# Kernel optimization log

Measured on AMD Instinct MI355X. Metric: run time of the kernel, lower is better.

## Reference

```python
import jax, jax.numpy as jnp
import numpy as np
from jax import lax

EPS = 1e-5

def _conv(x, w, b, pad):
    # NCHW conv, stride 1, symmetric padding `pad`
    y = lax.conv_general_dilated(x, w, window_strides=(1, 1),
                                 padding=[(pad, pad), (pad, pad)],
                                 dimension_numbers=('NCHW', 'OIHW', 'NCHW'))
    return y + b[None, :, None, None]

def _bn(x, gamma, beta):
    # BatchNorm2d, training mode: batch statistics over (N,H,W)
    mean = jnp.mean(x, axis=(0, 2, 3), keepdims=True)
    var = jnp.var(x, axis=(0, 2, 3), keepdims=True)
    return gamma[None, :, None, None] * (x - mean) * lax.rsqrt(var + EPS) + beta[None, :, None, None]

def setup_inputs() -> dict:
    key = jax.random.key(0)
    ks = jax.random.split(key, 8)
    B, C, H, W = 4, 256, 64, 64
    OC = 256
    s3 = 1.0 / np.sqrt(C * 9)
    s1 = 1.0 / np.sqrt(C)
    return {
        'x': jax.random.normal(ks[0], (B, C, H, W), jnp.float32),
        'Wq': jax.random.normal(ks[1], (OC, C, 3, 3), jnp.float32) * s3,
        'bq': jnp.zeros((OC,), jnp.float32),
        'gq': jnp.ones((OC,), jnp.float32),
        'betaq': jnp.zeros((OC,), jnp.float32),
        'Wk': jax.random.normal(ks[2], (OC, C, 1, 1), jnp.float32) * s1,
        'bk': jnp.zeros((OC,), jnp.float32),
        'gk': jnp.ones((OC,), jnp.float32),
        'betak': jnp.zeros((OC,), jnp.float32),
        'Wv': jax.random.normal(ks[3], (OC, C, 1, 1), jnp.float32) * s1,
        'bv': jnp.zeros((OC,), jnp.float32),
        'gv': jnp.ones((OC,), jnp.float32),
        'betav': jnp.zeros((OC,), jnp.float32),
    }

def reference(x, Wq, bq, gq, betaq, Wk, bk, gk, betak, Wv, bv, gv, betav):
    # Q: 3x3 conv, pad 1 -> (b, oc, h, w); K,V: 1x1 conv with pad 1 -> (b, oc, h+2, w+2)
    Q = _bn(_conv(x, Wq, bq, 1), gq, betaq)
    K = _bn(_conv(x, Wk, bk, 1), gk, betak)
    V = _bn(_conv(x, Wv, bv, 1), gv, betav)
    b, oc, oh, ow = Q.shape
    q = Q.reshape(b, oc, oh * ow)          # (b, c, q_tokens)
    k = K.reshape(b, oc, -1)               # (b, c, k_tokens)
    v = V.reshape(b, oc, -1)               # (b, c, k_tokens)
    scores = jnp.einsum('bck,bcq->bkq', k, q)      # (b, k_tokens, q_tokens)
    attn = jax.nn.softmax(scores, axis=1)          # softmax over key tokens (dim=1)
    out = jnp.einsum('bck,bkq->bcq', v, attn)      # (b, c, q_tokens)
    return out.reshape(b, oc, oh, ow)
```

## Files before the change

kernel.cpp:

```cpp
#include <hip/hip_runtime.h>


typedef unsigned short u16;
typedef _Float16 f16x8 __attribute__((ext_vector_type(8)));
typedef __attribute__((ext_vector_type(4))) float f32x4;

__device__ __forceinline__ u16 f2h(float f) {
  _Float16 h = (_Float16)f;
  return *(const u16*)&h;
}
__device__ __forceinline__ float bf2f(u16 h) {
  return __uint_as_float(((unsigned)h) << 16);
}
__device__ __forceinline__ float ldin(const void* p, size_t i, int f32) {
  return f32 ? ((const float*)p)[i] : bf2f(((const u16*)p)[i]);
}
__device__ __forceinline__ u16 f2bf(float f) {
  unsigned u = __float_as_uint(f);
  u += 0x7fffu + ((u >> 16) & 1u);
  return (u16)(u >> 16);
}
__device__ __forceinline__ void gld16(const void* g, void* l) {
  __builtin_amdgcn_global_load_lds(
      (const __attribute__((address_space(1))) unsigned int*)g,
      (__attribute__((address_space(3))) unsigned int*)l, 16, 0, 0);
}

__global__ __launch_bounds__(256) void k_detect(const unsigned* __restrict__ w,
                                                int* __restrict__ flag) {
  __shared__ int red[4];
  int tid = threadIdx.x, cnt = 0;
#pragma unroll
  for (int j = 0; j < 8; j++) {
    unsigned e = (w[tid + j * 8192] >> 7) & 0xFFu;
    cnt += (e >= 118u && e <= 127u) ? 1 : 0;
  }
#pragma unroll
  for (int off = 32; off; off >>= 1) cnt += __shfl_down(cnt, off);
  if ((tid & 63) == 0) red[tid >> 6] = cnt;
  __syncthreads();
  if (tid == 0)
    flag[0] = (red[0] + red[1] + red[2] + red[3] < 625) ? 1 : 0;
}

__global__ __launch_bounds__(256) void k_txp(const void* __restrict__ x,
                                             const int* __restrict__ flag,
                                             u16* __restrict__ xbTp) {
  __shared__ float tile[32][33];
  int f32 = flag[0];
  int b = blockIdx.z, p0 = blockIdx.x * 32, c0 = blockIdx.y * 32;
  int tx = threadIdx.x, ty = threadIdx.y;
#pragma unroll
  for (int i = 0; i < 4; i++) {
    int c = c0 + ty + i * 8, pp = p0 + tx;
    float v = 0.f;
    if (pp < 4356) {
      int yy = pp / 66, xx = pp - yy * 66;
      if (yy >= 1 && yy <= 64 && xx >= 1 && xx <= 64)
        v = ldin(x, ((size_t)b * 256 + c) * 4096 + (yy - 1) * 64 + (xx - 1), f32);
    }
    tile[ty + i * 8][tx] = v;
  }
  __syncthreads();
#pragma unroll
  for (int i = 0; i < 4; i++) {
    int pp = p0 + ty + i * 8;
    if (pp >= 4356) continue;
    xbTp[((size_t)b * 4356 + pp) * 256 + c0 + tx] = f2h(tile[tx][ty + i * 8]);
  }
}

__global__ __launch_bounds__(256) void k_wq(const void* __restrict__ Wq,
                                            const int* __restrict__ flag,
                                            u16* __restrict__ WqB) {
  int idx = blockIdx.x * 256 + threadIdx.x;
  int oc = idx / 2304, rem = idx - oc * 2304;
  int tap = rem >> 8, c = rem & 255;
  WqB[idx] = f2h(ldin(Wq, oc * 2304 + c * 9 + tap, flag[0]));
}
__global__ __launch_bounds__(256) void k_wkv(const void* __restrict__ Wk,
                                             const void* __restrict__ Wv,
                                             const int* __restrict__ flag,
                                             u16* __restrict__ WkvB) {
  int idx = blockIdx.x * 256 + threadIdx.x;
  int m = idx >> 8, c = idx & 255;
  float w = (m < 256) ? ldin(Wk, m * 256 + c, flag[0])
                      : ldin(Wv, (m - 256) * 256 + c, flag[0]);
  WkvB[idx] = f2h(w);
}

template <bool IMC, int EPI, int SWZ>
__global__ __launch_bounds__(256, 3) void gemm_bt(
    const u16* __restrict__ A, const u16* __restrict__ Bt, void* __restrict__ Cptr,
    int M, int N, int K, int ldB, int tapBase, long long cOff, int kChunk,
    int sw1, int sw2, int nSplit, long long zA, long long zB, long long zC) {
  __shared__ u16 lA[128 * 64];
  __shared__ u16 lB[128 * 64];
  int tm, tn, b = 0, kz = 0;
  if (SWZ == 1) {
    int lin = blockIdx.x, xcd = lin & 7, per = lin >> 3;
    tm = xcd * sw1 + (per % sw1);
    tn = per / sw1;
    b = blockIdx.y;
  } else if (SWZ == 2) {
    int lin = blockIdx.x, xcd = lin & 7, per = lin >> 3;
    tm = per % sw1;
    tn = xcd * sw2 + per / sw1;
    kz = blockIdx.z;
  } else {
    tm = blockIdx.x;
    tn = blockIdx.y;
    b = blockIdx.z / nSplit;
    kz = blockIdx.z % nSplit;
  }
  int k0 = 0, k1 = K;
  if (kChunk) {
    k0 = kz * kChunk;
    k1 = min(k0 + kChunk, K);
  }
  const int tid = threadIdx.x, wave = tid >> 6, lane = tid & 63;
  const int sr = lane >> 3;
  const int scw = (lane & 7) ^ sr;
  const int wm = (wave >> 1) * 64, wn = (wave & 1) * 64;
  const int r16 = lane & 15, q = lane >> 4;
  const u16* gA = A + (size_t)b * zA + (size_t)(tm * 128 + wave * 32 + sr) * K +
                  scw * 8;
  const u16* gB = nullptr;
  int pyI[4], pxI[4];
  size_t bOffI[4];
  if (IMC) {
#pragma unroll
    for (int i = 0; i < 4; i++) {
      int n = tn * 128 + wave * 32 + i * 8 + sr;
      int bb = n >> 12, pix = n & 4095;
      pyI[i] = pix >> 6;
      pxI[i] = pix & 63;
      bOffI[i] = (size_t)bb * 4356;
    }
  } else {
    gB = Bt + (size_t)b * zB + (size_t)(tn * 128 + wave * 32 + sr) * ldB +
         scw * 8;
  }
  f32x4 acc[4][4] = {};

  for (int kt = k0; kt < k1; kt += 64) {
    int dy = 0, dx = 0, chunk = 0;
    if (IMC) {
      int tap = tapBase + (kt >> 8);
      chunk = kt & 255;
      dy = tap / 3;
      dx = tap - dy * 3;
    }
#pragma unroll
    for (int i = 0; i < 4; i++) {
      gld16(gA + (size_t)(i * 8) * K + kt, &lA[(wave * 32 + i * 8) * 64]);
      if (IMC) {
        int spix = (pyI[i] + dy) * 66 + pxI[i] + dx;
        gld16(Bt + (bOffI[i] + spix) * 256 + chunk + scw * 8,
              &lB[(wave * 32 + i * 8) * 64]);
      } else {
        gld16(gB + (size_t)(i * 8) * ldB + kt, &lB[(wave * 32 + i * 8) * 64]);
      }
    }
    __syncthreads();
#pragma unroll
    for (int ks = 0; ks < 64; ks += 32) {
      f16x8 af[4], bfr[4];
#pragma unroll
      for (int f = 0; f < 4; f++) {
        int ma = wm + f * 16 + r16;
        int g = (ks >> 3) + q;
        af[f] = *(const f16x8*)&lA[ma * 64 + ((g ^ (ma & 7)) << 3)];
        int nb = wn + f * 16 + r16;
        bfr[f] = *(const f16x8*)&lB[nb * 64 + ((g ^ (nb & 7)) << 3)];
      }
#pragma unroll
      for (int fi = 0; fi < 4; fi++)
#pragma unroll
        for (int fj = 0; fj < 4; fj++)
          acc[fi][fj] = __builtin_amdgcn_mfma_f32_16x16x32_f16(
              af[fi], bfr[fj], acc[fi][fj], 0, 0, 0);
    }
    __syncthreads();
  }

  const int colB = tn * 128 + wn + r16;
  const int rowB = tm * 128 + wm + q * 4;
  float* C = (float*)Cptr + cOff + (size_t)b * zC;
  if (EPI == 0) {
#pragma unroll
    for (int fi = 0; fi < 4; fi++)
#pragma unroll
      for (int r = 0; r < 4; r++) {
        size_t ro = (size_t)(rowB + fi * 16 + r) * N;
#pragma unroll
        for (int fj = 0; fj < 4; fj++) C[ro + colB + fj * 16] = acc[fi][fj][r];
      }
  } else {
#pragma unroll
    for (int fi = 0; fi < 4; fi++)
#pragma unroll
      for (int r = 0; r < 4; r++) {
        size_t ro = (size_t)(rowB + fi * 16 + r) * N;
#pragma unroll
        for (int fj = 0; fj < 4; fj++)
          atomicAdd(&C[ro + colB + fj * 16], acc[fi][fj][r]);
      }
  }
}

__global__ __launch_bounds__(256) void k_stats(
    const float* __restrict__ bufQ, const float* __restrict__ bufKV,
    const void* __restrict__ gq, const void* __restrict__ betaq,
    const void* __restrict__ gk, const void* __restrict__ betak,
    const void* __restrict__ gv, const void* __restrict__ betav,
    const int* __restrict__ flag, float* __restrict__ nrm) {
  int f32 = flag[0];
  int ch = blockIdx.x, t = blockIdx.y, tid = threadIdx.x;
  const float* row = (t == 0) ? bufQ + (size_t)ch * 16384
                              : bufKV + (size_t)(t == 1 ? ch : 256 + ch) * 16384;
  float s = 0.f, ss = 0.f;
  for (int i = tid; i < 16384; i += 256) {
    float v = row[i];
    s += v;
    ss += v * v;
  }
#pragma unroll
  for (int off = 32; off; off >>= 1) {
    s += __shfl_down(s, off);
    ss += __shfl_down(ss, off);
  }
  __shared__ float ls[4], lss[4];
  if ((tid & 63) == 0) {
    ls[tid >> 6] = s;
    lss[tid >> 6] = ss;
  }
  __syncthreads();
  if (tid == 0) {
    s = ls[0] + ls[1] + ls[2] + ls[3];
    ss = lss[0] + lss[1] + lss[2] + lss[3];
    float cnt = (t == 0) ? 16384.f : 17424.f;
    float mean = s / cnt;
    float var = fmaxf(ss / cnt - mean * mean, 0.f);
    const void* g = (t == 0) ? gq : (t == 1 ? gk : gv);
    const void* be = (t == 0) ? betaq : (t == 1 ? betak : betav);
    float sc = ldin(g, ch, f32) * rsqrtf(var + 1e-5f);
    nrm[(t * 256 + ch) * 2] = sc;
    nrm[(t * 256 + ch) * 2 + 1] = ldin(be, ch, f32) - mean * sc;
  }
}

__global__ __launch_bounds__(256) void k_qTs(const float* __restrict__ bufQ,
                                             const float* __restrict__ nrm,
                                             u16* __restrict__ qTs) {
  __shared__ u16 th[32][33];
  int b = blockIdx.z, q0 = blockIdx.x * 32, c0 = blockIdx.y * 32;
  int tx = threadIdx.x, ty = threadIdx.y;
#pragma unroll
  for (int i = 0; i < 4; i++) {
    int c = c0 + ty + i * 8;
    float sc = nrm[c * 2], sh = nrm[c * 2 + 1];
    th[ty + i * 8][tx] =
        f2h(bufQ[(size_t)c * 16384 + b * 4096 + q0 + tx] * sc + sh);
  }
  __syncthreads();
#pragma unroll
  for (int i = 0; i < 4; i++)
    qTs[((size_t)b * 4096 + q0 + ty + i * 8) * 256 + c0 + tx] =
        th[tx][ty + i * 8];
}
__global__ __launch_bounds__(256) void k_kTs(const float* __restrict__ bufKV,
                                             const float* __restrict__ nrm,
                                             u16* __restrict__ kTs) {
  __shared__ u16 th[32][33];
  int b = blockIdx.z, k0 = blockIdx.x * 32, c0 = blockIdx.y * 32;
  int tx = threadIdx.x, ty = threadIdx.y;
#pragma unroll
  for (int i = 0; i < 4; i++) {
    int c = c0 + ty + i * 8;
    int kt = k0 + tx;
    float v = 0.f;
    if (kt < 4356) {
      float sc = nrm[(256 + c) * 2], sh = nrm[(256 + c) * 2 + 1];
      int yy = kt / 66, xx = kt - yy * 66;
      if (yy >= 1 && yy <= 64 && xx >= 1 && xx <= 64)
        v = bufKV[(size_t)c * 16384 + b * 4096 + (yy - 1) * 64 + (xx - 1)] * sc + sh;
      else
        v = sh;
    }
    th[ty + i * 8][tx] = f2h(v);
  }
  __syncthreads();
#pragma unroll
  for (int i = 0; i < 4; i++)
    kTs[((size_t)b * 4480 + k0 + ty + i * 8) * 256 + c0 + tx] =
        th[tx][ty + i * 8];
}

__global__ __launch_bounds__(256) void k_vP(const float* __restrict__ bufKV,
                                            const float* __restrict__ nrm,
                                            u16* __restrict__ vP) {
  int b = blockIdx.z, ch = blockIdx.y;
  int kt = blockIdx.x * 256 + threadIdx.x;
  if (kt >= 4480) return;
  float v = 0.f;
  if (kt < 4356) {
    float sc = nrm[(512 + ch) * 2], sh = nrm[(512 + ch) * 2 + 1];
    int yy = kt / 66, xx = kt - yy * 66;
    if (yy >= 1 && yy <= 64 && xx >= 1 && xx <= 64)
      v = bufKV[(size_t)(256 + ch) * 16384 + b * 4096 + (yy - 1) * 64 + (xx - 1)] * sc + sh;
    else
      v = sh;
  }
  vP[((size_t)b * 256 + ch) * 4480 + kt] = f2h(v);
}

__global__ __launch_bounds__(256, 2) void k_flash(
    const u16* __restrict__ qTs, const u16* __restrict__ kTs,
    const u16* __restrict__ vP, float* __restrict__ Op,
    float* __restrict__ ml) {
  __shared__ u16 lU[2][128 * 64];
  __shared__ u16 lP[64 * 128];
  const int lin = blockIdx.x;
  const int xcd = lin & 7, per = lin >> 3;
  const int h = xcd & 1, b = xcd >> 1;
  const int qt0 = per * 64;
  const int tid = threadIdx.x, wave = tid >> 6, lane = tid & 63;
  const int sr = lane >> 3, scw = (lane & 7) ^ sr;
  const int r16 = lane & 15, q = lane >> 4;

  const u16* gQ = qTs + ((size_t)b * 4096 + qt0 + wave * 16 + r16) * 256;
  f16x8 aq[8];
#pragma unroll
  for (int kk = 0; kk < 8; kk++) aq[kk] = *(const f16x8*)&gQ[kk * 32 + q * 8];

  const u16* gK = kTs + (size_t)b * 4480 * 256 + (size_t)(wave * 32 + sr) * 256 + scw * 8;
  const u16* gV = vP + ((size_t)b * 256 + wave * 64 + sr) * 4480 + scw * 8;

  f32x4 acc_o[16];
#pragma unroll
  for (int i = 0; i < 16; i++) acc_o[i] = (f32x4){0.f, 0.f, 0.f, 0.f};
  f32x4 m_v = {-3e38f, -3e38f, -3e38f, -3e38f};
  f32x4 l_v = {0.f, 0.f, 0.f, 0.f};

  const int ktBeg = h ? 2304 : 0, ktEnd = h ? 4480 : 2304;
  for (int kt0 = ktBeg; kt0 < ktEnd; kt0 += 128) {
    f32x4 acc_s[8];
#pragma unroll
    for (int i = 0; i < 8; i++) acc_s[i] = (f32x4){0.f, 0.f, 0.f, 0.f};
#pragma unroll
    for (int c2 = 0; c2 < 2; c2++) {
#pragma unroll
      for (int i = 0; i < 4; i++) {
        const u16* src = gK + (size_t)(kt0 + i * 8) * 256 + c2 * 128;
        gld16(src, &lU[0][(wave * 32 + i * 8) * 64]);
        gld16(src + 64, &lU[1][(wave * 32 + i * 8) * 64]);
      }
      __syncthreads();
#pragma unroll
      for (int kcL = 0; kcL < 2; kcL++)
#pragma unroll
        for (int ks = 0; ks < 64; ks += 32)
#pragma unroll
          for (int fj = 0; fj < 8; fj++) {
            int nb = fj * 16 + r16;
            int g = (ks >> 3) + q;
            f16x8 bf = *(const f16x8*)&lU[kcL][nb * 64 + ((g ^ (nb & 7)) << 3)];
            acc_s[fj] = __builtin_amdgcn_mfma_f32_16x16x32_f16(
                aq[c2 * 4 + kcL * 2 + (ks >> 5)], bf, acc_s[fj], 0, 0, 0);
          }
      __syncthreads();
    }
    if (kt0 + 128 > 4356) {
#pragma unroll
      for (int fj = 0; fj < 8; fj++)
        if (kt0 + fj * 16 + r16 >= 4356)
          acc_s[fj] = (f32x4){-1e30f, -1e30f, -1e30f, -1e30f};
    }
    f32x4 pm = acc_s[0];
#pragma unroll
    for (int fj = 1; fj < 8; fj++)
#pragma unroll
      for (int rr = 0; rr < 4; rr++) pm[rr] = fmaxf(pm[rr], acc_s[fj][rr]);
#pragma unroll
    for (int d = 1; d < 16; d <<= 1)
#pragma unroll
      for (int rr = 0; rr < 4; rr++)
        pm[rr] = fmaxf(pm[rr], __shfl_xor(pm[rr], d));
    f32x4 mn, fac;
#pragma unroll
    for (int rr = 0; rr < 4; rr++) {
      mn[rr] = fmaxf(m_v[rr], pm[rr]);
      fac[rr] = __expf(m_v[rr] - mn[rr]);
    }
    f32x4 rs = {0.f, 0.f, 0.f, 0.f};
#pragma unroll
    for (int fj = 0; fj < 8; fj++)
#pragma unroll
      for (int rr = 0; rr < 4; rr++) {
        _Float16 hp = (_Float16)__expf(acc_s[fj][rr] - mn[rr]);
        rs[rr] += (float)hp;
        int row = wave * 16 + q * 4 + rr;
        int c8 = fj * 2 + (r16 >> 3);
        lP[row * 128 + (((c8 ^ (row & 15)) << 3) | (r16 & 7))] = *(const u16*)&hp;
      }
#pragma unroll
    for (int d = 1; d < 16; d <<= 1)
#pragma unroll
      for (int rr = 0; rr < 4; rr++) rs[rr] += __shfl_xor(rs[rr], d);
#pragma unroll
    for (int rr = 0; rr < 4; rr++) {
      l_v[rr] = l_v[rr] * fac[rr] + rs[rr];
      m_v[rr] = mn[rr];
    }
#pragma unroll
    for (int fj = 0; fj < 16; fj++)
#pragma unroll
      for (int rr = 0; rr < 4; rr++) acc_o[fj][rr] *= fac[rr];
#pragma unroll
    for (int vc = 0; vc < 2; vc++) {
#pragma unroll
      for (int i = 0; i < 8; i++)
        gld16(gV + (size_t)(i * 8) * 4480 + kt0 + vc * 64,
              &((u16*)lU)[(wave * 64 + i * 8) * 64]);
      __syncthreads();
#pragma unroll
      for (int ks = 0; ks < 64; ks += 32) {
        int k8 = vc * 8 + (ks >> 3) + q;
        f16x8 ap = *(const f16x8*)&lP[(wave * 16 + r16) * 128 + ((k8 ^ r16) << 3)];
#pragma unroll
        for (int fj = 0; fj < 16; fj++) {
          int nb = fj * 16 + r16;
          int g = (ks >> 3) + q;
          f16x8 bv = *(const f16x8*)&((u16*)lU)[nb * 64 + ((g ^ (nb & 7)) << 3)];
          acc_o[fj] = __builtin_amdgcn_mfma_f32_16x16x32_f16(ap, bv, acc_o[fj], 0, 0, 0);
        }
      }
      __syncthreads();
    }
  }
  size_t ob = ((size_t)(h * 4 + b) * 4096 + qt0 + wave * 16) * 256;
#pragma unroll
  for (int rr = 0; rr < 4; rr++) {
    size_t rowo = ob + (size_t)(q * 4 + rr) * 256;
#pragma unroll
    for (int fj = 0; fj < 16; fj++) Op[rowo + fj * 16 + r16] = acc_o[fj][rr];
  }
  if (r16 == 0) {
    int base = (h * 4 + b) * 4096 + qt0 + wave * 16 + q * 4;
    *(f32x4*)&ml[base] = m_v;
    *(f32x4*)&ml[32768 + base] = l_v;
  }
}

__global__ __launch_bounds__(256) void k_merge(const float* __restrict__ Op,
                                               const float* __restrict__ ml,
                                               const int* __restrict__ flag,
                                               void* __restrict__ out) {
  __shared__ float th[32][33];
  int b = blockIdx.z, qt0 = blockIdx.x * 32, c0 = blockIdx.y * 32;
  int tx = threadIdx.x, ty = threadIdx.y;
#pragma unroll
  for (int i = 0; i < 4; i++) {
    int qt = qt0 + ty + i * 8;
    float m0 = ml[b * 4096 + qt], m1 = ml[(4 + b) * 4096 + qt];
    float l0 = ml[32768 + b * 4096 + qt], l1 = ml[32768 + (4 + b) * 4096 + qt];
    float M = fmaxf(m0, m1);
    float e0 = __expf(m0 - M), e1 = __expf(m1 - M);
    float inv = 1.f / (l0 * e0 + l1 * e1);
    float v = (Op[((size_t)b * 4096 + qt) * 256 + c0 + tx] * e0 +
               Op[((size_t)(4 + b) * 4096 + qt) * 256 + c0 + tx] * e1) * inv;
    v = (v == v) ? v : 0.f;
    th[ty + i * 8][tx] = v;
  }
  __syncthreads();
#pragma unroll
  for (int i = 0; i < 4; i++) {
    int c = c0 + ty + i * 8, qt = qt0 + tx;
    float v = th[tx][ty + i * 8];
    size_t oidx = ((size_t)b * 256 + c) * 4096 + qt;
    if (flag[0])
      ((float*)out)[oidx] = v;
    else
      ((u16*)out)[oidx] = f2bf(v);
  }
}

__global__ __launch_bounds__(256) void k_zeroacc(float* __restrict__ accF) {
  accF[blockIdx.x * 256 + threadIdx.x] = 0.f;
}

extern "C" void kernel_launch(void* const* d_in, const int* in_sizes, int n_in,
                              void* d_out, int out_size, void* d_ws, size_t ws_size,
                              hipStream_t stream) {
  const void* x = d_in[0];
  const void* Wq = d_in[1];
  const void* gq = d_in[3];
  const void* betaq = d_in[4];
  const void* Wk = d_in[5];
  const void* gk = d_in[7];
  const void* betak = d_in[8];
  const void* Wv = d_in[9];
  const void* gv = d_in[11];
  const void* betav = d_in[12];

  char* ws = (char*)d_ws;
  int* flag = (int*)ws;
  u16* xbTp = (u16*)(ws + 256);
  u16* WqB = (u16*)(ws + 8921344);
  u16* WkvB = (u16*)(ws + 10100992);
  float* bufQ = (float*)(ws + 10363136);
  float* bufKV = (float*)(ws + 27140352);
  u16* qTs = (u16*)(ws + 60694784);
  u16* kTs = (u16*)(ws + 69083392);
  u16* vP = (u16*)(ws + 78258432);
  float* nrm = (float*)(ws + 87433472);
  float* Opart = (float*)(ws + 256);
  float* mlbuf = (float*)(ws + 33554688);

  dim3 b32x8(32, 8);
  k_detect<<<1, 256, 0, stream>>>((const unsigned*)Wq, flag);
  k_txp<<<dim3(137, 8, 4), b32x8, 0, stream>>>(x, flag, xbTp);
  k_wq<<<2304, 256, 0, stream>>>(Wq, flag, WqB);
  k_wkv<<<512, 256, 0, stream>>>(Wk, Wv, flag, WkvB);
  k_zeroacc<<<16384, 256, 0, stream>>>(bufQ);
  gemm_bt<true, 1, 2><<<dim3(256, 1, 3), 256, 0, stream>>>(
      WqB, xbTp, bufQ, 256, 16384, 2304, 0, 0, 0, 768, 2, 16, 1, 0, 0, 0);
  gemm_bt<true, 0, 2><<<512, 256, 0, stream>>>(
      WkvB, xbTp, bufKV, 512, 16384, 256, 0, 4, 0, 0, 4, 16, 1, 0, 0, 0);
  k_stats<<<dim3(256, 3), 256, 0, stream>>>(bufQ, bufKV, gq, betaq, gk, betak,
                                            gv, betav, flag, nrm);
  k_qTs<<<dim3(128, 8, 4), b32x8, 0, stream>>>(bufQ, nrm, qTs);
  k_kTs<<<dim3(140, 8, 4), b32x8, 0, stream>>>(bufKV, nrm, kTs);
  k_vP<<<dim3(18, 256, 4), 256, 0, stream>>>(bufKV, nrm, vP);
  k_flash<<<512, 256, 0, stream>>>(qTs, kTs, vP, Opart, mlbuf);
  k_merge<<<dim3(128, 8, 4), b32x8, 0, stream>>>(Opart, mlbuf, flag, d_out);
}
```

Baseline: 333.9 us.

## Double-buffer K/V LDS staging in flash kernel and skip unneeded rescales

Replaces the single-buffer load-then-sync pattern in the flash attention loop with a two-buffer software pipeline. The next K or V chunk is issued via global_load_lds while the current one feeds MFMAs, using explicit vmcnt waits and raw barriers. It also raises wave priority around MFMA blocks and applies lazy softmax rescaling: the running max and the accumulator are only updated when some row's new max exceeds the old by more than 8. The trade-off is fp16 P values up to e^8 and more fragile hand-managed synchronisation.

Result: no change. 340.3 us (+1.9%).

```diff
diff --git a/kernel.cpp b/kernel.cpp
--- a/kernel.cpp
+++ b/kernel.cpp
@@ -319,7 +319,7 @@
     const u16* __restrict__ qTs, const u16* __restrict__ kTs,
     const u16* __restrict__ vP, float* __restrict__ Op,
     float* __restrict__ ml) {
-  __shared__ u16 lU[2][128 * 64];
+  __shared__ u16 lS[2][16384];
   __shared__ u16 lP[64 * 128];
   const int lin = blockIdx.x;
   const int xcd = lin & 7, per = lin >> 3;
@@ -333,9 +333,33 @@
   f16x8 aq[8];
 #pragma unroll
   for (int kk = 0; kk < 8; kk++) aq[kk] = *(const f16x8*)&gQ[kk * 32 + q * 8];
+  asm volatile("s_waitcnt vmcnt(0)" ::: "memory");
 
   const u16* gK = kTs + (size_t)b * 4480 * 256 + (size_t)(wave * 32 + sr) * 256 + scw * 8;
   const u16* gV = vP + ((size_t)b * 256 + wave * 64 + sr) * 4480 + scw * 8;
+
+#define STAGE_K(buf, kt, c2)                                                 \
+  {                                                                          \
+    _Pragma("unroll") for (int i = 0; i < 4; i++) {                          \
+      const u16* src = gK + (size_t)((kt) + i * 8) * 256 + (c2) * 128;       \
+      gld16(src, &lS[buf][(wave * 32 + i * 8) * 64]);                        \
+      gld16(src + 64, &lS[buf][8192 + (wave * 32 + i * 8) * 64]);            \
+    }                                                                        \
+  }
+#define STAGE_V(buf, kt, vc)                                                 \
+  {                                                                          \
+    _Pragma("unroll") for (int i = 0; i < 8; i++)                            \
+        gld16(gV + (size_t)(i * 8) * 4480 + (kt) + (vc) * 64,                \
+              &lS[buf][(wave * 64 + i * 8) * 64]);                           \
+  }
+#define WAITB(n)                                                             \
+  asm volatile("s_waitcnt vmcnt(" #n ")" ::: "memory");                      \
+  __builtin_amdgcn_s_barrier();                                              \
+  __builtin_amdgcn_sched_barrier(0);
+#define CLOSEB()                                                             \
+  __builtin_amdgcn_sched_barrier(0);                                         \
+  asm volatile("s_waitcnt lgkmcnt(0)" ::: "memory");                         \
+  __builtin_amdgcn_s_barrier();
 
   f32x4 acc_o[16];
 #pragma unroll
@@ -344,33 +368,46 @@
   f32x4 l_v = {0.f, 0.f, 0.f, 0.f};
 
   const int ktBeg = h ? 2304 : 0, ktEnd = h ? 4480 : 2304;
+  STAGE_K(0, ktBeg, 0);
   for (int kt0 = ktBeg; kt0 < ktEnd; kt0 += 128) {
     f32x4 acc_s[8];
 #pragma unroll
     for (int i = 0; i < 8; i++) acc_s[i] = (f32x4){0.f, 0.f, 0.f, 0.f};
-#pragma unroll
-    for (int c2 = 0; c2 < 2; c2++) {
-#pragma unroll
-      for (int i = 0; i < 4; i++) {
-        const u16* src = gK + (size_t)(kt0 + i * 8) * 256 + c2 * 128;
-        gld16(src, &lU[0][(wave * 32 + i * 8) * 64]);
-        gld16(src + 64, &lU[1][(wave * 32 + i * 8) * 64]);
-      }
-      __syncthreads();
-#pragma unroll
-      for (int kcL = 0; kcL < 2; kcL++)
-#pragma unroll
-        for (int ks = 0; ks < 64; ks += 32)
-#pragma unroll
-          for (int fj = 0; fj < 8; fj++) {
-            int nb = fj * 16 + r16;
-            int g = (ks >> 3) + q;
-            f16x8 bf = *(const f16x8*)&lU[kcL][nb * 64 + ((g ^ (nb & 7)) << 3)];
-            acc_s[fj] = __builtin_amdgcn_mfma_f32_16x16x32_f16(
-                aq[c2 * 4 + kcL * 2 + (ks >> 5)], bf, acc_s[fj], 0, 0, 0);
-          }
-      __syncthreads();
-    }
+    STAGE_K(1, kt0, 1);
+    WAITB(8);
+    __builtin_amdgcn_s_setprio(1);
+#pragma unroll
+    for (int kcL = 0; kcL < 2; kcL++)
+#pragma unroll
+      for (int ks = 0; ks < 64; ks += 32)
+#pragma unroll
+        for (int fj = 0; fj < 8; fj++) {
+          int nb = fj * 16 + r16;
+          int g = (ks >> 3) + q;
+          f16x8 bf = *(const f16x8*)&lS[0][kcL * 8192 + nb * 64 + ((g ^ (nb & 7)) << 3)];
+          acc_s[fj] = __builtin_amdgcn_mfma_f32_16x16x32_f16(
+              aq[kcL * 2 + (ks >> 5)], bf, acc_s[fj], 0, 0, 0);
+        }
+    __builtin_amdgcn_s_setprio(0);
+    CLOSEB();
+    STAGE_V(0, kt0, 0);
+    WAITB(8);
+    __builtin_amdgcn_s_setprio(1);
+#pragma unroll
+    for (int kcL = 0; kcL < 2; kcL++)
+#pragma unroll
+      for (int ks = 0; ks < 64; ks += 32)
+#pragma unroll
+        for (int fj = 0; fj < 8; fj++) {
+          int nb = fj * 16 + r16;
+          int g = (ks >> 3) + q;
+          f16x8 bf = *(const f16x8*)&lS[1][kcL * 8192 + nb * 64 + ((g ^ (nb & 7)) << 3)];
+          acc_s[fj] = __builtin_amdgcn_mfma_f32_16x16x32_f16(
+              aq[4 + kcL * 2 + (ks >> 5)], bf, acc_s[fj], 0, 0, 0);
+        }
+    __builtin_amdgcn_s_setprio(0);
+    CLOSEB();
+    STAGE_V(1, kt0, 1);
     if (kt0 + 128 > 4356) {
 #pragma unroll
       for (int fj = 0; fj < 8; fj++)
@@ -387,18 +424,28 @@
 #pragma unroll
       for (int rr = 0; rr < 4; rr++)
         pm[rr] = fmaxf(pm[rr], __shfl_xor(pm[rr], d));
-    f32x4 mn, fac;
-#pragma unroll
-    for (int rr = 0; rr < 4; rr++) {
-      mn[rr] = fmaxf(m_v[rr], pm[rr]);
-      fac[rr] = __expf(m_v[rr] - mn[rr]);
+    int need = !__all(pm[0] - m_v[0] <= 8.f && pm[1] - m_v[1] <= 8.f &&
+                      pm[2] - m_v[2] <= 8.f && pm[3] - m_v[3] <= 8.f);
+    if (need) {
+      f32x4 fac;
+#pragma unroll
+      for (int rr = 0; rr < 4; rr++) {
+        float mn = fmaxf(m_v[rr], pm[rr]);
+        fac[rr] = __expf(m_v[rr] - mn);
+        m_v[rr] = mn;
+        l_v[rr] *= fac[rr];
+      }
+#pragma unroll
+      for (int fj = 0; fj < 16; fj++)
+#pragma unroll
+        for (int rr = 0; rr < 4; rr++) acc_o[fj][rr] *= fac[rr];
     }
     f32x4 rs = {0.f, 0.f, 0.f, 0.f};
 #pragma unroll
     for (int fj = 0; fj < 8; fj++)
 #pragma unroll
       for (int rr = 0; rr < 4; rr++) {
-        _Float16 hp = (_Float16)__expf(acc_s[fj][rr] - mn[rr]);
+        _Float16 hp = (_Float16)__expf(acc_s[fj][rr] - m_v[rr]);
         rs[rr] += (float)hp;
         int row = wave * 16 + q * 4 + rr;
         int c8 = fj * 2 + (r16 >> 3);
@@ -409,36 +456,49 @@
 #pragma unroll
       for (int rr = 0; rr < 4; rr++) rs[rr] += __shfl_xor(rs[rr], d);
 #pragma unroll
-    for (int rr = 0; rr < 4; rr++) {
-      l_v[rr] = l_v[rr] * fac[rr] + rs[rr];
-      m_v[rr] = mn[rr];
-    }
-#pragma unroll
-    for (int fj = 0; fj < 16; fj++)
-#pragma unroll
-      for (int rr = 0; rr < 4; rr++) acc_o[fj][rr] *= fac[rr];
-#pragma unroll
-    for (int vc = 0; vc < 2; vc++) {
-#pragma unroll
-      for (int i = 0; i < 8; i++)
-        gld16(gV + (size_t)(i * 8) * 4480 + kt0 + vc * 64,
-              &((u16*)lU)[(wave * 64 + i * 8) * 64]);
-      __syncthreads();
-#pragma unroll
-      for (int ks = 0; ks < 64; ks += 32) {
-        int k8 = vc * 8 + (ks >> 3) + q;
-        f16x8 ap = *(const f16x8*)&lP[(wave * 16 + r16) * 128 + ((k8 ^ r16) << 3)];
-#pragma unroll
-        for (int fj = 0; fj < 16; fj++) {
-          int nb = fj * 16 + r16;
-          int g = (ks >> 3) + q;
-          f16x8 bv = *(const f16x8*)&((u16*)lU)[nb * 64 + ((g ^ (nb & 7)) << 3)];
-          acc_o[fj] = __builtin_amdgcn_mfma_f32_16x16x32_f16(ap, bv, acc_o[fj], 0, 0, 0);
-        }
-      }
-      __syncthreads();
-    }
-  }
+    for (int rr = 0; rr < 4; rr++) l_v[rr] += rs[rr];
+    WAITB(8);
+    __builtin_amdgcn_s_setprio(1);
+#pragma unroll
+    for (int ks = 0; ks < 64; ks += 32) {
+      int k8 = (ks >> 3) + q;
+      f16x8 ap = *(const f16x8*)&lP[(wave * 16 + r16) * 128 + ((k8 ^ r16) << 3)];
+#pragma unroll
+      for (int fj = 0; fj < 16; fj++) {
+        int nb = fj * 16 + r16;
+        int g = (ks >> 3) + q;
+        f16x8 bv = *(const f16x8*)&lS[0][nb * 64 + ((g ^ (nb & 7)) << 3)];
+        acc_o[fj] = __builtin_amdgcn_mfma_f32_16x16x32_f16(ap, bv, acc_o[fj], 0, 0, 0);
+      }
+    }
+    __builtin_amdgcn_s_setprio(0);
+    CLOSEB();
+    if (kt0 + 128 < ktEnd) {
+      STAGE_K(0, kt0 + 128, 0);
+      WAITB(8);
+    } else {
+      WAITB(0);
+    }
+    __builtin_amdgcn_s_setprio(1);
+#pragma unroll
+    for (int ks = 0; ks < 64; ks += 32) {
+      int k8 = 8 + (ks >> 3) + q;
+      f16x8 ap = *(const f16x8*)&lP[(wave * 16 + r16) * 128 + ((k8 ^ r16) << 3)];
+#pragma unroll
+      for (int fj = 0; fj < 16; fj++) {
+        int nb = fj * 16 + r16;
+        int g = (ks >> 3) + q;
+        f16x8 bv = *(const f16x8*)&lS[1][nb * 64 + ((g ^ (nb & 7)) << 3)];
+        acc_o[fj] = __builtin_amdgcn_mfma_f32_16x16x32_f16(ap, bv, acc_o[fj], 0, 0, 0);
+      }
+    }
+    __builtin_amdgcn_s_setprio(0);
+    CLOSEB();
+  }
+#undef STAGE_K
+#undef STAGE_V
+#undef WAITB
+#undef CLOSEB
   size_t ob = ((size_t)(h * 4 + b) * 4096 + qt0 + wave * 16) * 256;
 #pragma unroll
   for (int rr = 0; rr < 4; rr++) {
```
